# Optimization experiments

Hardware: AMD Instinct MI355X
Metric: run time of the kernel (lower is better)

Reference implementation:

```python
import math
import jax, jax.numpy as jnp
import numpy as np

B, S, D = 2, 2048, 1024
H = 8
HD = D // H // 2            # 64, per-branch head dim
ROT = HD // 2               # 32, rotary rot_dim (RotaryEmbedding dim=head_dim//2)
DEPTH = 2
LAMBDA_INIT = 0.8 - 0.6 * math.exp(-0.3 * DEPTH)


def rope(t):
    # t: (b, s, heads, HD); rotate first ROT dims with interleaved pairs
    s = t.shape[1]
    inv = 1.0 / (10000.0 ** (jnp.arange(0, ROT, 2, dtype=jnp.float32) / ROT))  # (ROT/2,)
    freqs = jnp.arange(s, dtype=jnp.float32)[:, None] * inv                    # (s, ROT/2)
    freqs = jnp.repeat(freqs, 2, axis=-1)                                      # (s, ROT)
    cos = jnp.cos(freqs)[None, :, None, :]
    sin = jnp.sin(freqs)[None, :, None, :]
    tl, tr = t[..., :ROT], t[..., ROT:]
    xp = tl.reshape(tl.shape[:-1] + (ROT // 2, 2))
    rh = jnp.stack((-xp[..., 1], xp[..., 0]), axis=-1).reshape(tl.shape)
    return jnp.concatenate([tl * cos + rh * sin, tr], axis=-1)


def rmsnorm(x, w, b, eps=1e-8):
    return x * jax.lax.rsqrt(jnp.mean(x * x, axis=-1, keepdims=True) + eps) * w + b


def layernorm(x, w, b, eps=1e-5):
    m = jnp.mean(x, axis=-1, keepdims=True)
    v = jnp.mean((x - m) ** 2, axis=-1, keepdims=True)
    return (x - m) * jax.lax.rsqrt(v + eps) * w + b


def causal_attn(q, k, v):
    # q,k: (b,s,h,dqk)  v: (b,s,h,dv) -> (b,s,h,dv); flash default scale 1/sqrt(dqk)
    s = q.shape[1]
    scores = jnp.einsum('bqhd,bkhd->bhqk', q, k) / jnp.sqrt(jnp.asarray(q.shape[-1], q.dtype))
    mask = jnp.tril(jnp.ones((s, s), dtype=bool))
    scores = jnp.where(mask, scores, jnp.asarray(-jnp.inf, scores.dtype))
    p = jax.nn.softmax(scores, axis=-1)
    return jnp.einsum('bhqk,bkhe->bqhe', p, v)


def setup_inputs() -> dict:
    key = jax.random.key(0)
    ks = jax.random.split(key, 16)
    f32 = jnp.float32
    inp = {
        'x': jax.random.normal(ks[0], (B, S, D), dtype=f32),
        'sigmas': jax.random.normal(ks[1], (B, HD), dtype=f32),
        'w_qkv': jax.random.normal(ks[2], (D, 3 * D), dtype=f32) * 0.02,
        'w_out': jax.random.normal(ks[3], (D, D), dtype=f32) * 0.02,
        'lq1': jax.random.normal(ks[4], (HD,), dtype=f32) * 0.1,
        'lk1': jax.random.normal(ks[5], (HD,), dtype=f32) * 0.1,
        'lq2': jax.random.normal(ks[6], (HD,), dtype=f32) * 0.1,
        'lk2': jax.random.normal(ks[7], (HD,), dtype=f32) * 0.1,
        'ln_w': jnp.ones((2 * HD,), f32) + 0.02 * jax.random.normal(ks[8], (2 * HD,), dtype=f32),
        'ln_b': 0.02 * jax.random.normal(ks[9], (2 * HD,), dtype=f32),
        'lnq_w': jnp.ones((HD,), f32) + 0.02 * jax.random.normal(ks[10], (HD,), dtype=f32),
        'lnq_b': 0.02 * jax.random.normal(ks[11], (HD,), dtype=f32),
        'ln1_w': jnp.ones((D,), f32), 'ln1_b': jnp.zeros((D,), f32),
        'ln2_w': jnp.ones((D,), f32), 'ln2_b': jnp.zeros((D,), f32),
        'w1': jax.random.normal(ks[12], (D, 4 * D), dtype=f32) * 0.02,
        'b1': jnp.zeros((4 * D,), f32),
        'w2': jax.random.normal(ks[13], (4 * D, D), dtype=f32) * 0.02,
        'b2': jnp.zeros((D,), f32),
    }
    return inp


def reference(x, sigmas, w_qkv, w_out, lq1, lk1, lq2, lk2, ln_w, ln_b,
              lnq_w, lnq_b, ln1_w, ln1_b, ln2_w, ln2_b, w1, b1, w2, b2):
    b, s, d = x.shape
    qkv = x @ w_qkv
    q, k, v = jnp.split(qkv, 3, axis=-1)
    q = q.reshape(b, s, 2 * H, HD)
    k = k.reshape(b, s, 2 * H, HD)
    v = v.reshape(b, s, H, 2 * HD)
    q = rope(q)
    k = rope(k)
    q = q.reshape(b, s, H, 2, HD)
    k = k.reshape(b, s, H, 2, HD)
    q1, q2 = q[..., 0, :], q[..., 1, :]
    k1, k2 = k[..., 0, :], k[..., 1, :]
    sig = sigmas[:, None, None, :]  # (b,1,1,HD)
    attn1 = causal_attn(q1, k1, v)
    attn2 = causal_attn(rmsnorm(q2 + sig, lnq_w, lnq_b), rmsnorm(k2 + sig, lnq_w, lnq_b), v)
    lam = jnp.exp(jnp.sum(lq1 * lk1)) - jnp.exp(jnp.sum(lq2 * lk2)) + LAMBDA_INIT
    a = rmsnorm(attn1 - lam * attn2, ln_w, ln_b) * (1.0 - LAMBDA_INIT)
    a = a.reshape(b, s, d) @ w_out
    h = layernorm(a + x, ln1_w, ln1_b)
    ff = jax.nn.silu(h @ w1 + b1) @ w2 + b2
    return layernorm(ff + h, ln2_w, ln2_b)
```

## Files before the change

### kernel.cpp

```cpp
#include <hip/hip_runtime.h>
#include <math.h>
#include <stdint.h>

#define B_ 2
#define S_ 2048
#define D_ 1024
#define H_ 8
#define NT_ (B_*S_)

static constexpr float LAMBDA_INIT = 0.47071301834358415f;
static constexpr float ONE_MINUS_LI = 1.0f - 0.47071301834358415f;

typedef __attribute__((ext_vector_type(8))) short bf16x8;
typedef __attribute__((ext_vector_type(4))) float f32x4;

__device__ __forceinline__ unsigned short f2bf(float x) {
    union { float f; unsigned int u; } v; v.f = x;
    unsigned int r = v.u + 0x7fffu + ((v.u >> 16) & 1u);
    return (unsigned short)(r >> 16);
}
__device__ __forceinline__ float bf2f(unsigned short b) {
    union { unsigned int u; float f; } v; v.u = ((unsigned int)b) << 16;
    return v.f;
}

#define GLD16(gp, lp) __builtin_amdgcn_global_load_lds( \
    (const __attribute__((address_space(1))) void*)(gp), \
    (__attribute__((address_space(3))) void*)(lp), 16, 0, 0)

__global__ void lam_kernel(const float* __restrict__ lq1, const float* __restrict__ lk1,
                           const float* __restrict__ lq2, const float* __restrict__ lk2,
                           float* __restrict__ lam_out) {
    int t = threadIdx.x;
    float p1 = lq1[t] * lk1[t];
    float p2 = lq2[t] * lk2[t];
    for (int off = 32; off; off >>= 1) {
        p1 += __shfl_xor(p1, off);
        p2 += __shfl_xor(p2, off);
    }
    if (t == 0) lam_out[0] = expf(p1) - expf(p2) + LAMBDA_INIT;
}

__global__ __launch_bounds__(256) void prep_kernel(const float* __restrict__ x,
                                                   const float* __restrict__ w_qkv,
                                                   const float* __restrict__ w_out,
                                                   const float* __restrict__ w1,
                                                   const float* __restrict__ w2,
                                                   short* __restrict__ x_bf,
                                                   short* __restrict__ w_qkvT,
                                                   short* __restrict__ w_outT,
                                                   short* __restrict__ w1T,
                                                   short* __restrict__ w2T) {
    const int z = blockIdx.x;
    if (z >= 12288) {
        const size_t i = ((size_t)(z - 12288) * 256 + threadIdx.x) * 4;
        float4 v = *(const float4*)(x + i);
        *(ushort4*)(x_bf + i) = make_ushort4(f2bf(v.x), f2bf(v.y), f2bf(v.z), f2bf(v.w));
        return;
    }
    const float* W; short* WT; int K, N, zz;
    if (z < 3072)      { W = w_qkv; WT = w_qkvT; K = 1024; N = 3072; zz = z; }
    else if (z < 4096) { W = w_out; WT = w_outT; K = 1024; N = 1024; zz = z - 3072; }
    else if (z < 8192) { W = w1;    WT = w1T;    K = 1024; N = 4096; zz = z - 4096; }
    else               { W = w2;    WT = w2T;    K = 4096; N = 1024; zz = z - 8192; }
    const int nx = N >> 5;
    const int bx = zz % nx, by = zz / nx;
    __shared__ float tile[32][33];
    const int t = threadIdx.x;
    const int k0 = by * 32, n0 = bx * 32;
    const int r = t >> 3, c0 = (t & 7) * 4;
    float4 v = *(const float4*)(W + (size_t)(k0 + r) * N + n0 + c0);
    tile[r][c0 + 0] = v.x; tile[r][c0 + 1] = v.y;
    tile[r][c0 + 2] = v.z; tile[r][c0 + 3] = v.w;
    __syncthreads();
    ushort4 o = make_ushort4(f2bf(tile[c0 + 0][r]), f2bf(tile[c0 + 1][r]),
                             f2bf(tile[c0 + 2][r]), f2bf(tile[c0 + 3][r]));
    *(ushort4*)(WT + (size_t)(n0 + r) * K + k0 + c0) = o;
}

__global__ __launch_bounds__(256) void vtrans_kernel(const short* __restrict__ qkv_bf,
                                                     short* __restrict__ vt) {
    __shared__ short tile[32][34];
    const int s0 = blockIdx.x * 32, e0 = blockIdx.y * 32, bh = blockIdx.z;
    const int b = bh >> 3, h = bh & 7;
    const int t = threadIdx.x, r = t >> 3, c0 = (t & 7) * 4;
    ushort4 v = *(const ushort4*)(qkv_bf + (size_t)(b * S_ + s0 + r) * 3072 + 2048 + h * 128 + e0 + c0);
    tile[r][c0 + 0] = v.x; tile[r][c0 + 1] = v.y;
    tile[r][c0 + 2] = v.z; tile[r][c0 + 3] = v.w;
    __syncthreads();
    ushort4 o = make_ushort4((unsigned short)tile[c0 + 0][r], (unsigned short)tile[c0 + 1][r],
                             (unsigned short)tile[c0 + 2][r], (unsigned short)tile[c0 + 3][r]);
    *(ushort4*)(vt + ((size_t)bh * 128 + e0 + r) * S_ + s0 + c0) = o;
}

template <int EPI, int OUTBF, int SPLITK>
__global__ __launch_bounds__(256) void gemm_bt(const short* __restrict__ A,
                                               const short* __restrict__ BT,
                                               const float* __restrict__ bias,
                                               void* __restrict__ C0,
                                               void* __restrict__ C1,
                                               int M, int N, int Kfull, int Ksub) {
    __shared__ short As[3][128 * 32];
    __shared__ short Bs[3][128 * 32];
    const int t = threadIdx.x;
    const int w = t >> 6, l = t & 63;
    const int lr = l & 15, lg = l >> 4;

    const int GX = gridDim.x;
    const int nwg = GX * gridDim.y;
    int flat = blockIdx.y * GX + blockIdx.x;
    flat = (flat & 7) * (nwg >> 3) + (flat >> 3);
    int part = 0;
    if (SPLITK) { const int per = nwg >> 1; part = flat / per; flat = flat % per; }
    const int per_part = SPLITK ? (nwg >> 1) : nwg;
    const int GYp = per_part / GX;
    const int panel = flat / (8 * GYp);
    const int idx = flat % (8 * GYp);
    const int by = idx >> 3;
    const int bx = panel * 8 + (idx & 7);
    const int row0 = by * 128, col0 = bx * 128;
    const int wr = (w >> 1) * 64, wc = (w & 1) * 64;

    f32x4 acc[4][4];
#pragma unroll
    for (int i = 0; i < 4; ++i)
#pragma unroll
        for (int j = 0; j < 4; ++j) acc[i][j] = (f32x4){0.f, 0.f, 0.f, 0.f};

    const int sg = ((l & 3) ^ ((l >> 3) & 3)) * 8;
    const short* Ag = A + (size_t)part * Ksub + (size_t)(row0 + w * 32 + (l >> 2)) * Kfull + sg;
    const short* Bg = BT + (size_t)part * Ksub + (size_t)(col0 + w * 32 + (l >> 2)) * Kfull + sg;

    const int nst = Ksub >> 5;

    auto stage = [&](int T, int Bf) {
#pragma unroll
        for (int j = 0; j < 2; ++j) {
            GLD16(Ag + (T << 5) + (size_t)j * 16 * Kfull, &As[Bf][(w * 2 + j) * 512]);
            GLD16(Bg + (T << 5) + (size_t)j * 16 * Kfull, &Bs[Bf][(w * 2 + j) * 512]);
        }
    };

    stage(0, 0);
    stage(1, 1);

    const int rslot = (lg ^ ((lr >> 1) & 3)) * 8;

    int cur = 0;
    for (int k = 0; k < nst; ++k) {
        if (k + 1 < nst) {
            asm volatile("s_waitcnt vmcnt(4)" ::: "memory");
        } else {
            asm volatile("s_waitcnt vmcnt(0)" ::: "memory");
        }
        __builtin_amdgcn_s_barrier();
        __builtin_amdgcn_sched_barrier(0);
        const int nk = k + 2;
        if (nk < nst) {
            int nb = cur + 2; if (nb >= 3) nb -= 3;
            stage(nk, nb);
        }
        bf16x8 af[4], bfr[4];
#pragma unroll
        for (int i = 0; i < 4; ++i)
            af[i] = *(const bf16x8*)(&As[cur][(wr + i * 16 + lr) * 32 + rslot]);
#pragma unroll
        for (int j = 0; j < 4; ++j)
            bfr[j] = *(const bf16x8*)(&Bs[cur][(wc + j * 16 + lr) * 32 + rslot]);
#pragma unroll
        for (int i = 0; i < 4; ++i)
#pragma unroll
            for (int j = 0; j < 4; ++j)
                acc[i][j] = __builtin_amdgcn_mfma_f32_16x16x32_bf16(af[i], bfr[j], acc[i][j], 0, 0, 0);
        __builtin_amdgcn_sched_barrier(0);
        asm volatile("s_waitcnt lgkmcnt(0)" ::: "memory");
        cur = (cur + 1 == 3) ? 0 : cur + 1;
    }

    void* Cout = (SPLITK && part) ? C1 : C0;
#pragma unroll
    for (int i = 0; i < 4; ++i) {
#pragma unroll
        for (int j = 0; j < 4; ++j) {
            const int col = col0 + wc + j * 16 + lr;
            float bcol = (EPI >= 1) ? bias[col] : 0.f;
#pragma unroll
            for (int r = 0; r < 4; ++r) {
                const int row = row0 + wr + i * 16 + lg * 4 + r;
                float v = acc[i][j][r];
                if (EPI >= 1) v += bcol;
                if (EPI == 2) v = v / (1.0f + expf(-v));
                if (OUTBF) ((short*)Cout)[(size_t)row * N + col] = (short)f2bf(v);
                else       ((float*)Cout)[(size_t)row * N + col] = v;
            }
        }
    }
}

__global__ __launch_bounds__(256) void rope_kernel(const short* __restrict__ qkv,
                                                   const float* __restrict__ sigmas,
                                                   const float* __restrict__ lnq_w,
                                                   const float* __restrict__ lnq_b,
                                                   short* __restrict__ q1, short* __restrict__ q2n,
                                                   short* __restrict__ k1, short* __restrict__ k2n) {
    const int tok = blockIdx.x;
    const int b = tok >> 11, s = tok & 2047;
    const int t = threadIdx.x;
    const int hh = t >> 4;
    const int d0 = (t & 15) * 4;

    const short* qrow = qkv + (size_t)tok * 3072 + hh * 64 + d0;
    ushort4 qv = *(const ushort4*)qrow;
    ushort4 kv = *(const ushort4*)(qrow + 1024);
    float q[4] = {bf2f(qv.x), bf2f(qv.y), bf2f(qv.z), bf2f(qv.w)};
    float k[4] = {bf2f(kv.x), bf2f(kv.y), bf2f(kv.z), bf2f(kv.w)};

    if (d0 < 32) {
#pragma unroll
        for (int pr = 0; pr < 2; ++pr) {
            const int i = d0 / 2 + pr;
            float freq = (float)s * powf(10000.0f, -(float)i / 16.0f);
            float sn, c;
            sincosf(freq, &sn, &c);
            float x0 = q[2 * pr], x1 = q[2 * pr + 1];
            q[2 * pr]     = x0 * c - x1 * sn;
            q[2 * pr + 1] = x1 * c + x0 * sn;
            x0 = k[2 * pr]; x1 = k[2 * pr + 1];
            k[2 * pr]     = x0 * c - x1 * sn;
            k[2 * pr + 1] = x1 * c + x0 * sn;
        }
    }

    const int h = hh >> 1, j = hh & 1;
    const size_t obase = ((size_t)(b * H_ + h) * S_ + s) * 64 + d0;
    if (j == 0) {
        *(ushort4*)&q1[obase] = make_ushort4(f2bf(q[0]), f2bf(q[1]), f2bf(q[2]), f2bf(q[3]));
        *(ushort4*)&k1[obase] = make_ushort4(f2bf(k[0]), f2bf(k[1]), f2bf(k[2]), f2bf(k[3]));
    } else {
        float ssq_q = 0.f, ssq_k = 0.f;
#pragma unroll
        for (int i = 0; i < 4; ++i) {
            const float sg = sigmas[b * 64 + d0 + i];
            q[i] += sg; k[i] += sg;
            ssq_q += q[i] * q[i];
            ssq_k += k[i] * k[i];
        }
        for (int off = 1; off < 16; off <<= 1) {
            ssq_q += __shfl_xor(ssq_q, off, 16);
            ssq_k += __shfl_xor(ssq_k, off, 16);
        }
        const float rq = rsqrtf(ssq_q / 64.0f + 1e-8f);
        const float rk = rsqrtf(ssq_k / 64.0f + 1e-8f);
        float oq[4], ok[4];
#pragma unroll
        for (int i = 0; i < 4; ++i) {
            const float w = lnq_w[d0 + i], bb = lnq_b[d0 + i];
            oq[i] = q[i] * rq * w + bb;
            ok[i] = k[i] * rk * w + bb;
        }
        *(ushort4*)&q2n[obase] = make_ushort4(f2bf(oq[0]), f2bf(oq[1]), f2bf(oq[2]), f2bf(oq[3]));
        *(ushort4*)&k2n[obase] = make_ushort4(f2bf(ok[0]), f2bf(ok[1]), f2bf(ok[2]), f2bf(ok[3]));
    }
}

__device__ __forceinline__ void sm_update(f32x4 (&s)[4], float (&m)[4], float (&lsum)[4],
                                          f32x4 (&o)[8], short* __restrict__ Pw,
                                          const bool diag, const int qr0, const int k0,
                                          const int lr, const int lg) {
    float nm[4];
#pragma unroll
    for (int r = 0; r < 4; ++r) nm[r] = m[r];
#pragma unroll
    for (int ks = 0; ks < 4; ++ks) {
#pragma unroll
        for (int r = 0; r < 4; ++r) {
            float v = s[ks][r];
            if (diag && (k0 + ks * 16 + lr > qr0 + r)) v = -INFINITY;
            else v *= 0.125f;
            s[ks][r] = v;
            nm[r] = fmaxf(nm[r], v);
        }
    }
#pragma unroll
    for (int r = 0; r < 4; ++r) {
        nm[r] = fmaxf(nm[r], __shfl_xor(nm[r], 1));
        nm[r] = fmaxf(nm[r], __shfl_xor(nm[r], 2));
        nm[r] = fmaxf(nm[r], __shfl_xor(nm[r], 4));
        nm[r] = fmaxf(nm[r], __shfl_xor(nm[r], 8));
    }
    bool grow = false;
#pragma unroll
    for (int r = 0; r < 4; ++r) grow = grow || (nm[r] > m[r] + 8.0f);
    if (__any(grow)) {
        float al[4];
#pragma unroll
        for (int r = 0; r < 4; ++r) {
            al[r] = __expf(m[r] - nm[r]);
            m[r] = nm[r];
            lsum[r] *= al[r];
        }
#pragma unroll
        for (int es = 0; es < 8; ++es) {
#pragma unroll
            for (int r = 0; r < 4; ++r) o[es][r] *= al[r];
        }
    }
    float rs[4] = {0.f, 0.f, 0.f, 0.f};
#pragma unroll
    for (int ks = 0; ks < 4; ++ks) {
#pragma unroll
        for (int r = 0; r < 4; ++r) {
            float p = __expf(s[ks][r] - m[r]);
            rs[r] += p;
            Pw[(lg * 4 + r) * 72 + ks * 16 + lr] = (short)f2bf(p);
        }
    }
#pragma unroll
    for (int r = 0; r < 4; ++r) {
        rs[r] += __shfl_xor(rs[r], 1);
        rs[r] += __shfl_xor(rs[r], 2);
        rs[r] += __shfl_xor(rs[r], 4);
        rs[r] += __shfl_xor(rs[r], 8);
        lsum[r] += rs[r];
    }
}

__global__ __launch_bounds__(256, 3) void attn_part(const short* __restrict__ q1g,
                                                    const short* __restrict__ q2g,
                                                    const short* __restrict__ k1g,
                                                    const short* __restrict__ k2g,
                                                    const short* __restrict__ vt,
                                                    short* __restrict__ pO0,
                                                    short* __restrict__ pO1,
                                                    float* __restrict__ pml) {
    __shared__ short Ks1[64 * 72];
    __shared__ short Ks2[64 * 72];
    __shared__ short Vt[128 * 72];
    __shared__ short Ps[4][16 * 72];

    const int i = blockIdx.x;
    const int xcd = i & 7;
    const int slot = i >> 3;
    const int a = slot >> 6;
    const int j = slot & 63;
    const int qt = 31 - (j >> 1);
    const int part = j & 1;
    const int bh = xcd * 2 + a;
    const int q0 = qt * 64;
    const int t = threadIdx.x, w = t >> 6, l = t & 63;
    const int lr = l & 15, lg = l >> 4;

    const size_t kbase = (size_t)bh * S_ * 64;
    const size_t vbase = (size_t)bh * 128 * S_;

    bf16x8 qa1[2], qa2[2];
    {
        const size_t rb = kbase + (size_t)(q0 + w * 16 + lr) * 64;
#pragma unroll
        for (int dh = 0; dh < 2; ++dh) {
            qa1[dh] = *(const bf16x8*)(q1g + rb + dh * 32 + lg * 8);
            qa2[dh] = *(const bf16x8*)(q2g + rb + dh * 32 + lg * 8);
        }
    }

    const int nkt = qt + 1, mid = (nkt + 1) >> 1;
    const int kt0 = part ? mid : 0, kt1 = part ? nkt : mid;

    float m1[4], m2[4], l1[4], l2[4];
#pragma unroll
    for (int r = 0; r < 4; ++r) { m1[r] = -1e30f; m2[r] = -1e30f; l1[r] = 0.f; l2[r] = 0.f; }
    f32x4 o1[8], o2[8];
#pragma unroll
    for (int es = 0; es < 8; ++es) { o1[es] = (f32x4){0.f,0.f,0.f,0.f}; o2[es] = (f32x4){0.f,0.f,0.f,0.f}; }

    short* Pw = &Ps[w][0];
    const int qr0 = q0 + w * 16 + lg * 4;
    const int wrow_lo = q0 + w * 16;

    const int sr = t >> 2, sc = (t & 3) * 16;
    const int vr = t >> 1, vc = (t & 1) * 32;

    for (int kt = kt0; kt < kt1; ++kt) {
        const int k0 = kt * 64;
        __syncthreads();
        {
            const size_t g = kbase + (size_t)(k0 + sr) * 64 + sc;
            *(bf16x8*)(Ks1 + sr * 72 + sc)     = *(const bf16x8*)(k1g + g);
            *(bf16x8*)(Ks1 + sr * 72 + sc + 8) = *(const bf16x8*)(k1g + g + 8);
            *(bf16x8*)(Ks2 + sr * 72 + sc)     = *(const bf16x8*)(k2g + g);
            *(bf16x8*)(Ks2 + sr * 72 + sc + 8) = *(const bf16x8*)(k2g + g + 8);
            const size_t gv = vbase + (size_t)vr * S_ + k0 + vc;
#pragma unroll
            for (int jj = 0; jj < 4; ++jj)
                *(bf16x8*)(Vt + vr * 72 + vc + jj * 8) = *(const bf16x8*)(vt + gv + jj * 8);
        }
        __syncthreads();

        const bool diag = (k0 + 63 > wrow_lo);

        {
            f32x4 s[4];
#pragma unroll
            for (int ks = 0; ks < 4; ++ks) s[ks] = (f32x4){0.f,0.f,0.f,0.f};
            __builtin_amdgcn_s_setprio(1);
#pragma unroll
            for (int ks = 0; ks < 4; ++ks)
#pragma unroll
                for (int dh = 0; dh < 2; ++dh) {
                    bf16x8 kf = *(const bf16x8*)(Ks1 + (ks * 16 + lr) * 72 + dh * 32 + lg * 8);
                    s[ks] = __builtin_amdgcn_mfma_f32_16x16x32_bf16(qa1[dh], kf, s[ks], 0, 0, 0);
                }
            __builtin_amdgcn_s_setprio(0);
            sm_update(s, m1, l1, o1, Pw, diag, qr0, k0, lr, lg);
            __builtin_amdgcn_s_setprio(1);
#pragma unroll
            for (int kb = 0; kb < 2; ++kb) {
                bf16x8 pf = *(const bf16x8*)(Pw + lr * 72 + kb * 32 + lg * 8);
#pragma unroll
                for (int es = 0; es < 8; ++es) {
                    bf16x8 vf = *(const bf16x8*)(Vt + (es * 16 + lr) * 72 + kb * 32 + lg * 8);
                    o1[es] = __builtin_amdgcn_mfma_f32_16x16x32_bf16(pf, vf, o1[es], 0, 0, 0);
                }
            }
            __builtin_amdgcn_s_setprio(0);
        }
        {
            f32x4 s[4];
#pragma unroll
            for (int ks = 0; ks < 4; ++ks) s[ks] = (f32x4){0.f,0.f,0.f,0.f};
            __builtin_amdgcn_s_setprio(1);
#pragma unroll
            for (int ks = 0; ks < 4; ++ks)
#pragma unroll
                for (int dh = 0; dh < 2; ++dh) {
                    bf16x8 kf = *(const bf16x8*)(Ks2 + (ks * 16 + lr) * 72 + dh * 32 + lg * 8);
                    s[ks] = __builtin_amdgcn_mfma_f32_16x16x32_bf16(qa2[dh], kf, s[ks], 0, 0, 0);
                }
            __builtin_amdgcn_s_setprio(0);
            sm_update(s, m2, l2, o2, Pw, diag, qr0, k0, lr, lg);
            __builtin_amdgcn_s_setprio(1);
#pragma unroll
            for (int kb = 0; kb < 2; ++kb) {
                bf16x8 pf = *(const bf16x8*)(Pw + lr * 72 + kb * 32 + lg * 8);
#pragma unroll
                for (int es = 0; es < 8; ++es) {
                    bf16x8 vf = *(const bf16x8*)(Vt + (es * 16 + lr) * 72 + kb * 32 + lg * 8);
                    o2[es] = __builtin_amdgcn_mfma_f32_16x16x32_bf16(pf, vf, o2[es], 0, 0, 0);
                }
            }
            __builtin_amdgcn_s_setprio(0);
        }
    }

    {
        uint32_t* pO = (uint32_t*)(part ? pO1 : pO0);
        const size_t wb = (((size_t)bh * 32 + qt) * 4 + w) * 2048;
#pragma unroll
        for (int r = 0; r < 4; ++r) {
#pragma unroll
            for (int u = 0; u < 4; ++u) {
                uint32_t v1 = (uint32_t)f2bf(o1[2 * u][r]) | ((uint32_t)f2bf(o1[2 * u + 1][r]) << 16);
                pO[wb + (size_t)((r * 2 + 0) * 4 + u) * 64 + l] = v1;
                uint32_t v2 = (uint32_t)f2bf(o2[2 * u][r]) | ((uint32_t)f2bf(o2[2 * u + 1][r]) << 16);
                pO[wb + (size_t)((r * 2 + 1) * 4 + u) * 64 + l] = v2;
            }
        }
    }
    if (lr == 0) {
#pragma unroll
        for (int r = 0; r < 4; ++r) {
            const int q = q0 + w * 16 + lg * 4 + r;
            float4 v = make_float4(m1[r], l1[r], m2[r], l2[r]);
            *(float4*)&pml[(((size_t)part * 16 + bh) * S_ + q) * 4] = v;
        }
    }
}

__global__ __launch_bounds__(256) void attn_combine(const short* __restrict__ pO0,
                                                    const short* __restrict__ pO1,
                                                    const float* __restrict__ pml,
                                                    const float* __restrict__ lamp,
                                                    const float* __restrict__ ln_w,
                                                    const float* __restrict__ ln_b,
                                                    short* __restrict__ arms) {
    const int tok = blockIdx.x;
    const int b = tok >> 11, q = tok & 2047;
    const int t = threadIdx.x;
    const int h = t >> 5, ln32 = t & 31, e0 = ln32 * 4;
    const int bh = b * H_ + h;
    const float lam = lamp[0];

    float4 mla = *(const float4*)&pml[(((size_t)0 * 16 + bh) * S_ + q) * 4];
    float4 mlb = *(const float4*)&pml[(((size_t)1 * 16 + bh) * S_ + q) * 4];

    const float m1 = fmaxf(mla.x, mlb.x);
    const float aa1 = __expf(mla.x - m1), ab1 = __expf(mlb.x - m1);
    const float il1 = 1.0f / (aa1 * mla.y + ab1 * mlb.y);
    const float m2 = fmaxf(mla.z, mlb.z);
    const float aa2 = __expf(mla.z - m2), ab2 = __expf(mlb.z - m2);
    const float il2 = 1.0f / (aa2 * mla.w + ab2 * mlb.w);

    const int qt = q >> 6, w = (q >> 4) & 3, lg = (q >> 2) & 3, r = q & 3;
    const int es = ln32 >> 2, u = es >> 1, half = es & 1;
    const int lane0 = lg * 16 + (ln32 & 3) * 4;
    const size_t wb = (((size_t)bh * 32 + qt) * 4 + w) * 2048;
    const uint32_t* P0 = (const uint32_t*)pO0;
    const uint32_t* P1 = (const uint32_t*)pO1;
    const uint4 a1  = *(const uint4*)&P0[wb + (size_t)((r * 2 + 0) * 4 + u) * 64 + lane0];
    const uint4 b1v = *(const uint4*)&P1[wb + (size_t)((r * 2 + 0) * 4 + u) * 64 + lane0];
    const uint4 a2  = *(const uint4*)&P0[wb + (size_t)((r * 2 + 1) * 4 + u) * 64 + lane0];
    const uint4 b2v = *(const uint4*)&P1[wb + (size_t)((r * 2 + 1) * 4 + u) * 64 + lane0];
    const int sh = 16 * half;

    float comb[4]; float ssq = 0.f;
    {
        const uint32_t aw1[4] = {a1.x, a1.y, a1.z, a1.w};
        const uint32_t bw1[4] = {b1v.x, b1v.y, b1v.z, b1v.w};
        const uint32_t aw2[4] = {a2.x, a2.y, a2.z, a2.w};
        const uint32_t bw2[4] = {b2v.x, b2v.y, b2v.z, b2v.w};
#pragma unroll
        for (int i = 0; i < 4; ++i) {
            const float O1 = (aa1 * bf2f((unsigned short)(aw1[i] >> sh)) +
                              ab1 * bf2f((unsigned short)(bw1[i] >> sh))) * il1;
            const float O2 = (aa2 * bf2f((unsigned short)(aw2[i] >> sh)) +
                              ab2 * bf2f((unsigned short)(bw2[i] >> sh))) * il2;
            const float c = O1 - lam * O2;
            comb[i] = c; ssq += c * c;
        }
    }
    for (int off = 1; off < 32; off <<= 1) ssq += __shfl_xor(ssq, off, 32);
    const float rms = rsqrtf(ssq / 128.0f + 1e-8f);

    ushort4 o;
    unsigned short* op = (unsigned short*)&o;
#pragma unroll
    for (int i = 0; i < 4; ++i) {
        const int e = e0 + i;
        op[i] = f2bf((comb[i] * rms * ln_w[e] + ln_b[e]) * ONE_MINUS_LI);
    }
    *(ushort4*)&arms[(size_t)tok * 1024 + h * 128 + e0] = o;
}

__global__ __launch_bounds__(256) void add_ln1_kernel(const float* __restrict__ A0,
                                                      const float* __restrict__ A1,
                                                      const float* __restrict__ X,
                                                      const float* __restrict__ w,
                                                      const float* __restrict__ bvec,
                                                      short* __restrict__ out_bf) {
    const int row = blockIdx.x;
    const int t = threadIdx.x;
    __shared__ float red[4];

    float4 a0 = *(const float4*)&A0[(size_t)row * 1024 + t * 4];
    float4 a1 = *(const float4*)&A1[(size_t)row * 1024 + t * 4];
    float4 xv = *(const float4*)&X[(size_t)row * 1024 + t * 4];
    float v[4] = {a0.x + a1.x + xv.x, a0.y + a1.y + xv.y,
                  a0.z + a1.z + xv.z, a0.w + a1.w + xv.w};

    float s = v[0] + v[1] + v[2] + v[3];
    for (int off = 1; off < 64; off <<= 1) s += __shfl_xor(s, off);
    if ((t & 63) == 0) red[t >> 6] = s;
    __syncthreads();
    const float mean = (red[0] + red[1] + red[2] + red[3]) * (1.0f / 1024.0f);

    float sq = 0.f;
#pragma unroll
    for (int i = 0; i < 4; ++i) { const float d = v[i] - mean; sq += d * d; }
    __syncthreads();
    for (int off = 1; off < 64; off <<= 1) sq += __shfl_xor(sq, off);
    if ((t & 63) == 0) red[t >> 6] = sq;
    __syncthreads();
    const float var = (red[0] + red[1] + red[2] + red[3]) * (1.0f / 1024.0f);
    const float rstd = rsqrtf(var + 1e-5f);

    ushort4 o;
    unsigned short* op = (unsigned short*)&o;
#pragma unroll
    for (int i = 0; i < 4; ++i)
        op[i] = f2bf((v[i] - mean) * rstd * w[t * 4 + i] + bvec[t * 4 + i]);
    *(ushort4*)&out_bf[(size_t)row * 1024 + t * 4] = o;
}

__global__ __launch_bounds__(256) void add_ln2_kernel(const float* __restrict__ F0,
                                                      const float* __restrict__ F1,
                                                      const float* __restrict__ bias,
                                                      const short* __restrict__ Hbf,
                                                      const float* __restrict__ w,
                                                      const float* __restrict__ bvec,
                                                      float* __restrict__ out) {
    const int row = blockIdx.x;
    const int t = threadIdx.x;
    __shared__ float red[4];

    float4 f0 = *(const float4*)&F0[(size_t)row * 1024 + t * 4];
    float4 f1 = *(const float4*)&F1[(size_t)row * 1024 + t * 4];
    float4 bv = *(const float4*)&bias[t * 4];
    ushort4 hv = *(const ushort4*)&Hbf[(size_t)row * 1024 + t * 4];
    float v[4] = {f0.x + f1.x + bv.x + bf2f(hv.x), f0.y + f1.y + bv.y + bf2f(hv.y),
                  f0.z + f1.z + bv.z + bf2f(hv.z), f0.w + f1.w + bv.w + bf2f(hv.w)};

    float s = v[0] + v[1] + v[2] + v[3];
    for (int off = 1; off < 64; off <<= 1) s += __shfl_xor(s, off);
    if ((t & 63) == 0) red[t >> 6] = s;
    __syncthreads();
    const float mean = (red[0] + red[1] + red[2] + red[3]) * (1.0f / 1024.0f);

    float sq = 0.f;
#pragma unroll
    for (int i = 0; i < 4; ++i) { const float d = v[i] - mean; sq += d * d; }
    __syncthreads();
    for (int off = 1; off < 64; off <<= 1) sq += __shfl_xor(sq, off);
    if ((t & 63) == 0) red[t >> 6] = sq;
    __syncthreads();
    const float var = (red[0] + red[1] + red[2] + red[3]) * (1.0f / 1024.0f);
    const float rstd = rsqrtf(var + 1e-5f);

    float o[4];
#pragma unroll
    for (int i = 0; i < 4; ++i)
        o[i] = (v[i] - mean) * rstd * w[t * 4 + i] + bvec[t * 4 + i];
    *(float4*)&out[(size_t)row * 1024 + t * 4] = make_float4(o[0], o[1], o[2], o[3]);
}

extern "C" void kernel_launch(void* const* d_in, const int* in_sizes, int n_in,
                              void* d_out, int out_size, void* d_ws, size_t ws_size,
                              hipStream_t stream) {
    const float* x      = (const float*)d_in[0];
    const float* sigmas = (const float*)d_in[1];
    const float* w_qkv  = (const float*)d_in[2];
    const float* w_out  = (const float*)d_in[3];
    const float* lq1    = (const float*)d_in[4];
    const float* lk1    = (const float*)d_in[5];
    const float* lq2    = (const float*)d_in[6];
    const float* lk2    = (const float*)d_in[7];
    const float* ln_w   = (const float*)d_in[8];
    const float* ln_b   = (const float*)d_in[9];
    const float* lnq_w  = (const float*)d_in[10];
    const float* lnq_b  = (const float*)d_in[11];
    const float* ln1_w  = (const float*)d_in[12];
    const float* ln1_b  = (const float*)d_in[13];
    const float* ln2_w  = (const float*)d_in[14];
    const float* ln2_b  = (const float*)d_in[15];
    const float* w1     = (const float*)d_in[16];
    const float* b1     = (const float*)d_in[17];
    const float* w2     = (const float*)d_in[18];
    const float* b2     = (const float*)d_in[19];

    char* ws = (char*)d_ws;
    short* x_bf    = (short*)(ws + 0);
    short* vt      = (short*)(ws + 0);
    short* h_bf    = (short*)(ws + 0);
    short* w_qkvT  = (short*)(ws + 8388608);
    short* w_outT  = (short*)(ws + 14680064);
    short* w1T     = (short*)(ws + 16777216);
    short* w2T     = (short*)(ws + 25165824);
    short* qkv_bf  = (short*)(ws + 33554432);
    short* pO0     = (short*)(ws + 33554432);
    float* pml     = (float*)(ws + 50331648);
    float* a_p0    = (float*)(ws + 33554432);
    short* q1      = (short*)(ws + 58720256);
    short* q2n     = (short*)(ws + 62914560);
    short* k1      = (short*)(ws + 67108864);
    short* k2n     = (short*)(ws + 71303168);
    float* a_p1    = (float*)(ws + 58720256);
    short* pO1     = (short*)(ws + 75497472);
    short* arms    = (short*)(ws + 92274688);
    short* ffh     = (short*)(ws + 33554432);
    float* ff_p0   = (float*)(ws + 67108864);
    float* ff_p1   = (float*)(ws + 83886080);
    float* lam     = (float*)(ws + 100663296);

    lam_kernel<<<1, 64, 0, stream>>>(lq1, lk1, lq2, lk2, lam);
    prep_kernel<<<16384, 256, 0, stream>>>(x, w_qkv, w_out, w1, w2,
                                           x_bf, w_qkvT, w_outT, w1T, w2T);

    gemm_bt<0, 1, 0><<<dim3(24, 32), 256, 0, stream>>>(x_bf, w_qkvT, nullptr,
                                                       qkv_bf, nullptr, NT_, 3072, 1024, 1024);

    rope_kernel<<<NT_, 256, 0, stream>>>(qkv_bf, sigmas, lnq_w, lnq_b, q1, q2n, k1, k2n);
    vtrans_kernel<<<dim3(S_ / 32, 4, 16), 256, 0, stream>>>(qkv_bf, vt);

    attn_part<<<1024, 256, 0, stream>>>(q1, q2n, k1, k2n, vt, pO0, pO1, pml);
    attn_combine<<<NT_, 256, 0, stream>>>(pO0, pO1, pml, lam, ln_w, ln_b, arms);

    gemm_bt<0, 0, 1><<<dim3(8, 64), 256, 0, stream>>>(arms, w_outT, nullptr,
                                                      a_p0, a_p1, NT_, 1024, 1024, 512);

    add_ln1_kernel<<<NT_, 256, 0, stream>>>(a_p0, a_p1, x, ln1_w, ln1_b, h_bf);

    gemm_bt<2, 1, 0><<<dim3(32, 32), 256, 0, stream>>>(h_bf, w1T, b1,
                                                       ffh, nullptr, NT_, 4096, 1024, 1024);

    gemm_bt<0, 0, 1><<<dim3(8, 64), 256, 0, stream>>>(ffh, w2T, nullptr,
                                                      ff_p0, ff_p1, NT_, 1024, 4096, 2048);

    add_ln2_kernel<<<NT_, 256, 0, stream>>>(ff_p0, ff_p1, b2, h_bf, ln2_w, ln2_b,
                                            (float*)d_out);
}
```

Measured before the change: 320.1 us.

## Add 256x256-tile 512-thread GEMM for QKV and FFN1 projections

Introduces a new bf16 MFMA GEMM kernel with 256x256 output tiles, 8 waves per block, and double-buffered 64-wide K stages in LDS. It also remaps block indices across XCD-sized groups. It replaces the 128-tile GEMM for the QKV projection and the bias+SiLU FFN1 projection, aiming for more operand reuse per LDS load and fewer global reads. The trade-offs are a much smaller grid (192 blocks for QKV, fewer than the CU count), a large LDS footprint that likely allows only one block per CU, and high register pressure from 32 accumulators per thread.

```diff
diff --git a/kernel.cpp b/kernel.cpp
--- a/kernel.cpp
+++ b/kernel.cpp
@@ -192,6 +192,92 @@
                 if (EPI == 2) v = v / (1.0f + expf(-v));
                 if (OUTBF) ((short*)Cout)[(size_t)row * N + col] = (short)f2bf(v);
                 else       ((float*)Cout)[(size_t)row * N + col] = v;
+            }
+        }
+    }
+}
+
+template <int EPI>
+__global__ __launch_bounds__(512, 2) void gemm256(const short* __restrict__ A,
+                                                  const short* __restrict__ BT,
+                                                  const float* __restrict__ bias,
+                                                  short* __restrict__ Cout,
+                                                  int M, int N, int K) {
+    __shared__ short As[2][256 * 64];
+    __shared__ short Bs[2][256 * 64];
+    const int t = threadIdx.x;
+    const int w = t >> 6, l = t & 63;
+    const int lr = l & 15, lg = l >> 4;
+
+    const int GX = gridDim.x;
+    const int nwg = GX * gridDim.y;
+    int flat = blockIdx.y * GX + blockIdx.x;
+    flat = (flat & 7) * (nwg >> 3) + (flat >> 3);
+    const int bx = flat % GX, by = flat / GX;
+    const int row0 = by * 256, col0 = bx * 256;
+    const int wr = (w >> 2) * 128, wc = (w & 3) * 64;
+
+    f32x4 acc[8][4];
+#pragma unroll
+    for (int i = 0; i < 8; ++i)
+#pragma unroll
+        for (int j = 0; j < 4; ++j) acc[i][j] = (f32x4){0.f, 0.f, 0.f, 0.f};
+
+    const int sg = (((l & 7) ^ ((l >> 3) & 7))) * 8;
+    const short* Ag = A + (size_t)(row0 + w * 32 + (l >> 3)) * K + sg;
+    const short* Bg = BT + (size_t)(col0 + w * 32 + (l >> 3)) * K + sg;
+
+    const int nst = K >> 6;
+
+    auto stage = [&](int T, int Bf) {
+#pragma unroll
+        for (int j = 0; j < 4; ++j) {
+            GLD16(Ag + (T << 6) + (size_t)j * 8 * K, &As[Bf][(w * 4 + j) * 512]);
+            GLD16(Bg + (T << 6) + (size_t)j * 8 * K, &Bs[Bf][(w * 4 + j) * 512]);
+        }
+    };
+
+    stage(0, 0);
+    __syncthreads();
+
+    int cur = 0;
+    for (int k = 0; k < nst; ++k) {
+        if (k + 1 < nst) stage(k + 1, cur ^ 1);
+        __builtin_amdgcn_s_setprio(1);
+#pragma unroll
+        for (int kk = 0; kk < 2; ++kk) {
+            const int rs = ((kk * 4 + lg) ^ (lr & 7)) * 8;
+            bf16x8 af[8], bfr[4];
+#pragma unroll
+            for (int i = 0; i < 8; ++i)
+                af[i] = *(const bf16x8*)(&As[cur][(wr + i * 16 + lr) * 64 + rs]);
+#pragma unroll
+            for (int j = 0; j < 4; ++j)
+                bfr[j] = *(const bf16x8*)(&Bs[cur][(wc + j * 16 + lr) * 64 + rs]);
+#pragma unroll
+            for (int i = 0; i < 8; ++i)
+#pragma unroll
+                for (int j = 0; j < 4; ++j)
+                    acc[i][j] = __builtin_amdgcn_mfma_f32_16x16x32_bf16(af[i], bfr[j], acc[i][j], 0, 0, 0);
+        }
+        __builtin_amdgcn_s_setprio(0);
+        __syncthreads();
+        cur ^= 1;
+    }
+
+#pragma unroll
+    for (int i = 0; i < 8; ++i) {
+#pragma unroll
+        for (int j = 0; j < 4; ++j) {
+            const int col = col0 + wc + j * 16 + lr;
+            float bcol = (EPI >= 1) ? bias[col] : 0.f;
+#pragma unroll
+            for (int r = 0; r < 4; ++r) {
+                const int row = row0 + wr + i * 16 + lg * 4 + r;
+                float v = acc[i][j][r];
+                if (EPI >= 1) v += bcol;
+                if (EPI == 2) v = v / (1.0f + expf(-v));
+                Cout[(size_t)row * N + col] = (short)f2bf(v);
             }
         }
     }
@@ -674,8 +760,8 @@
     prep_kernel<<<16384, 256, 0, stream>>>(x, w_qkv, w_out, w1, w2,
                                            x_bf, w_qkvT, w_outT, w1T, w2T);
 
-    gemm_bt<0, 1, 0><<<dim3(24, 32), 256, 0, stream>>>(x_bf, w_qkvT, nullptr,
-                                                       qkv_bf, nullptr, NT_, 3072, 1024, 1024);
+    gemm256<0><<<dim3(12, 16), 512, 0, stream>>>(x_bf, w_qkvT, nullptr,
+                                                 qkv_bf, NT_, 3072, 1024);
 
     rope_kernel<<<NT_, 256, 0, stream>>>(qkv_bf, sigmas, lnq_w, lnq_b, q1, q2n, k1, k2n);
     vtrans_kernel<<<dim3(S_ / 32, 4, 16), 256, 0, stream>>>(qkv_bf, vt);
@@ -688,8 +774,8 @@
 
     add_ln1_kernel<<<NT_, 256, 0, stream>>>(a_p0, a_p1, x, ln1_w, ln1_b, h_bf);
 
-    gemm_bt<2, 1, 0><<<dim3(32, 32), 256, 0, stream>>>(h_bf, w1T, b1,
-                                                       ffh, nullptr, NT_, 4096, 1024, 1024);
+    gemm256<2><<<dim3(16, 16), 512, 0, stream>>>(h_bf, w1T, b1,
+                                                 ffh, NT_, 4096, 1024);
 
     gemm_bt<0, 0, 1><<<dim3(8, 64), 256, 0, stream>>>(ffh, w2T, nullptr,
                                                       ff_p0, ff_p1, NT_, 1024, 4096, 2048);
```

New measurement: 315.1 us (median of 2 runs). Within noise of the previous version (-1.6%).
